# Performance work log

Measured on AMD Instinct MI355X. Metric: run time of the kernel, lower is better.

The kernel has to match this reference:

```python
import jax, jax.numpy as jnp
import numpy as np
import math

# Model hyperparameters (SchNet defaults)
H = 128        # hidden_channels
F = 128        # num_filters
G = 50         # num_gaussians
CUT = 6.0      # cutoff (Angstrom)
L_INT = 3      # num_interactions
# Graph scale
N_MOL = 512    # molecules
APM = 32       # atoms per molecule
N = N_MOL * APM
BOX = 10.0     # side of cubic box per molecule


def _ssp(x):
    # ShiftedSoftplus
    return jax.nn.softplus(x) - math.log(2.0)


def setup_inputs() -> dict:
    rng = np.random.default_rng(0)
    pos = rng.uniform(0.0, BOX, (N_MOL, APM, 3)).astype(np.float32)
    # radius graph within each molecule (faithful to radius_graph_custom,
    # precomputed here because edge count is data-dependent)
    srcs, dsts = [], []
    for m in range(N_MOL):
        p = pos[m]
        dm = np.linalg.norm(p[:, None, :] - p[None, :, :], axis=-1)
        mask = dm <= CUT
        np.fill_diagonal(mask, False)
        s, t = np.nonzero(mask)
        srcs.append(s + m * APM)
        dsts.append(t + m * APM)
    edge_index = np.stack([np.concatenate(srcs), np.concatenate(dsts)]).astype(np.int32)
    pos = pos.reshape(N, 3)
    batch = np.repeat(np.arange(N_MOL, dtype=np.int32), APM)
    z = rng.integers(1, 100, N).astype(np.int32)

    key = jax.random.key(0)
    ks = jax.random.split(key, 16)
    s = 0.1
    nrm = lambda k, shp: (jax.random.normal(k, shp, dtype=jnp.float32) * s)
    return {
        "z": jnp.asarray(z),
        "pos": jnp.asarray(pos),
        "batch": jnp.asarray(batch),
        "edge_index": jnp.asarray(edge_index),
        "emb": nrm(ks[0], (100, H)),
        "mlp_w1": nrm(ks[1], (L_INT, G, F)),
        "mlp_b1": jnp.zeros((L_INT, F), jnp.float32),
        "mlp_w2": nrm(ks[2], (L_INT, F, F)),
        "mlp_b2": jnp.zeros((L_INT, F), jnp.float32),
        "cf1_w": nrm(ks[3], (L_INT, H, F)),
        "cf2_w": nrm(ks[4], (L_INT, F, H)),
        "cf2_b": jnp.zeros((L_INT, H), jnp.float32),
        "lin_w": nrm(ks[5], (L_INT, H, H)),
        "lin_b": jnp.zeros((L_INT, H), jnp.float32),
        "out1_w": nrm(ks[6], (H, H // 2)),
        "out1_b": jnp.zeros((H // 2,), jnp.float32),
        "out2_w": nrm(ks[7], (H // 2, 1)),
        "out2_b": jnp.zeros((1,), jnp.float32),
    }


def reference(z, pos, batch, edge_index, emb,
              mlp_w1, mlp_b1, mlp_w2, mlp_b2,
              cf1_w, cf2_w, cf2_b, lin_w, lin_b,
              out1_w, out1_b, out2_w, out2_b):
    src, dst = edge_index[0], edge_index[1]
    # edge_weight = euclidean distance (== cdist[src, dst])
    d = jnp.sqrt(jnp.sum((pos[src] - pos[dst]) ** 2, axis=-1))  # [E]
    # GaussianSmearing
    offs = jnp.linspace(0.0, CUT, G)
    coeff = -0.5 / (CUT / (G - 1)) ** 2
    edge_attr = jnp.exp(coeff * (d[:, None] - offs[None, :]) ** 2)  # [E, G]
    # cosine cutoff
    Ccut = 0.5 * (jnp.cos(d * math.pi / CUT) + 1.0)  # [E]

    h = emb[z]  # [N, H]
    for l in range(L_INT):
        # edge filter MLP with cutoff
        W = _ssp(edge_attr @ mlp_w1[l] + mlp_b1[l]) @ mlp_w2[l] + mlp_b2[l]  # [E, F]
        W = W * Ccut[:, None]
        # CFConv: lin1 -> gather x_j -> multiply -> scatter-add to dst -> lin2
        msg = (h @ cf1_w[l])[src] * W                                # [E, F]
        agg = jax.ops.segment_sum(msg, dst, num_segments=N)          # [N, F]
        v = agg @ cf2_w[l] + cf2_b[l]                                # [N, H]
        v = _ssp(v)
        v = v @ lin_w[l] + lin_b[l]
        h = h + v  # residual

    h = _ssp(h @ out1_w + out1_b)
    h = h @ out2_w + out2_b                                          # [N, 1]
    out = jax.ops.segment_sum(h, batch, num_segments=N_MOL)          # [N_MOL, 1]
    return out
```

## Files before the change

kernel.cpp:

```cpp
#include <hip/hip_runtime.h>
#include <hip/hip_bf16.h>
#include <math.h>

#define NATOMS 16384
#define NMOL   512
#define APM    32
#define GDIM   50
#define KTAB   4096
#define MAXEPM 1000

#define STRH 132
#define STRA 136

typedef __attribute__((ext_vector_type(8))) short   short8;
typedef __attribute__((ext_vector_type(4))) float   floatx4;

__device__ __forceinline__ float ssp(float x) {
    float e = __expf(-fabsf(x));
    return fmaxf(x, 0.0f) + __logf(1.0f + e) - 0.69314718055994531f;
}

__device__ __forceinline__ unsigned short f2bf(float x) {
    union { float f; unsigned int u; } v; v.f = x;
    unsigned int lsb = (v.u >> 16) & 1u;
    v.u += 0x7fffu + lsb;
    return (unsigned short)(v.u >> 16);
}

__device__ __forceinline__ unsigned int pk2bf(float a, float b) {
    __hip_bfloat162 h = __float22bfloat162_rn(make_float2(a, b));
    unsigned int u;
    __builtin_memcpy(&u, &h, 4);
    return u;
}

#define KW1 72
#define KW2 136
#define NTILE (KTAB / 64)

__global__ __launch_bounds__(256) void mega_setup_kernel(
    const float* __restrict__ pos, const int* __restrict__ eidx, int E, int EB,
    int* __restrict__ rowptr,
    const float* __restrict__ cf1, const float* __restrict__ cf2,
    const float* __restrict__ lin, const float* __restrict__ out1,
    unsigned short* __restrict__ Wtall, unsigned int* __restrict__ meta,
    const float* __restrict__ w1_, const float* __restrict__ b1_,
    const float* __restrict__ w2_, const float* __restrict__ b2_,
    unsigned short* __restrict__ Tt)
{
    const int WB = (9 * 16384 + 64 * 128 + 255) / 256;
    const int b = blockIdx.x;
    const int tid = threadIdx.x;

    if (b < EB) {
        int idx = b * 256 + tid;
        if (idx < E) {
            int s = eidx[idx], t = eidx[E + idx];
            float dx = pos[3 * s]     - pos[3 * t];
            float dy = pos[3 * s + 1] - pos[3 * t + 1];
            float dz = pos[3 * s + 2] - pos[3 * t + 2];
            float d  = sqrtf(dx * dx + dy * dy + dz * dz);
            float u  = d * (float)(KTAB - 1) / 6.0f;
            int i = min((int)(u + 0.5f), KTAB - 1);
            meta[idx] = ((unsigned)i << 6) | (unsigned)(t & 31);
        } else if (idx < E + NATOMS + 1) {
            int a = idx - E;
            int lo = 0, hi = E;
            while (lo < hi) { int mid = (lo + hi) >> 1; if (eidx[mid] < a) lo = mid + 1; else hi = mid; }
            rowptr[a] = lo;
        }
        return;
    }
    if (b < EB + WB) {
        int idx = (b - EB) * 256 + tid;
        if (idx < 9 * 16384) {
            int wi = idx >> 14, rem = idx & 16383;
            int n = rem >> 7, k = rem & 127;
            int l = wi / 3, which = wi % 3;
            const float* src = (which == 0) ? cf1 : (which == 1) ? cf2 : lin;
            Wtall[idx] = f2bf(src[(size_t)l * 16384 + k * 128 + n]);
        } else if (idx < 9 * 16384 + 64 * 128) {
            int q = idx - 9 * 16384;
            int n = q >> 7, k = q & 127;
            Wtall[idx] = f2bf(out1[k * 64 + n]);
        }
        return;
    }

    __shared__ unsigned short s_bufA[128 * KW2];
    __shared__ unsigned short s_bufB[128 * KW1];

    const int tt = b - EB - WB;
    const int l  = tt / NTILE;
    const int bx = tt % NTILE;
    const float* w1 = w1_ + (size_t)l * GDIM * 128;
    const float* b1 = b1_ + (size_t)l * 128;
    const float* w2 = w2_ + (size_t)l * 128 * 128;
    const float* b2 = b2_ + (size_t)l * 128;
    unsigned short* Tg = Tt + (size_t)l * KTAB * 128;

    unsigned short* s_w1T = s_bufB;
    unsigned short* s_w2T = s_bufA;
    unsigned short* s_t   = s_bufB;

    for (int i = tid; i < GDIM * 128; i += 256) {
        int g = i >> 7, f = i & 127;
        s_w1T[f * KW1 + g] = f2bf(w1[i]);
    }
    for (int i = tid; i < (64 - GDIM) * 128; i += 256) {
        int g = GDIM + (i >> 7), f = i & 127;
        s_w1T[f * KW1 + g] = 0;
    }
    for (int i = tid; i < 128 * 128; i += 256) {
        int k = i >> 7, n = i & 127;
        s_w2T[n * KW2 + k] = f2bf(w2[i]);
    }

    const int lane = tid & 63;
    const int w    = tid >> 6;
    const int l15  = lane & 15;
    const int quad = lane >> 4;

    float b1v[8], b2v[8];
    #pragma unroll
    for (int nt = 0; nt < 8; nt++) {
        b1v[nt] = b1[nt * 16 + l15];
        b2v[nt] = b2[nt * 16 + l15];
    }
    __syncthreads();

    const float hstep = 6.0f / (float)(KTAB - 1);
    const float step  = 6.0f / 49.0f;
    const float coeff = -0.5f / (step * step);
    const float pioc  = 3.14159265358979323846f / 6.0f;
    const int k0 = bx * 64;
    const float dm = (float)(k0 + w * 16 + l15) * hstep;

    floatx4 acc1[8];
    #pragma unroll
    for (int nt = 0; nt < 8; nt++) acc1[nt] = (floatx4){0.f, 0.f, 0.f, 0.f};
    #pragma unroll
    for (int ks = 0; ks < 2; ks++) {
        unsigned int ap[4];
        #pragma unroll
        for (int jj = 0; jj < 4; jj++) {
            int g0 = ks * 32 + quad * 8 + 2 * jj;
            float d0 = dm - (float)g0 * step;
            float d1 = dm - (float)(g0 + 1) * step;
            float v0 = (g0 < GDIM)     ? __expf(coeff * d0 * d0) : 0.0f;
            float v1 = (g0 + 1 < GDIM) ? __expf(coeff * d1 * d1) : 0.0f;
            ap[jj] = pk2bf(v0, v1);
        }
        short8 af;
        __builtin_memcpy(&af, ap, 16);
        #pragma unroll
        for (int nt = 0; nt < 8; nt++) {
            short8 bfg = *(const short8*)&s_w1T[(nt * 16 + l15) * KW1 + ks * 32 + quad * 8];
            acc1[nt] = __builtin_amdgcn_mfma_f32_16x16x32_bf16(af, bfg, acc1[nt], 0, 0, 0);
        }
    }
    __syncthreads();

    #pragma unroll
    for (int nt = 0; nt < 8; nt++) {
        #pragma unroll
        for (int r = 0; r < 4; r++) {
            int row = w * 16 + quad * 4 + r;
            s_t[row * KW2 + nt * 16 + l15] = f2bf(ssp(acc1[nt][r] + b1v[nt]));
        }
    }

    floatx4 acc2[8];
    #pragma unroll
    for (int nt = 0; nt < 8; nt++) acc2[nt] = (floatx4){0.f, 0.f, 0.f, 0.f};
    #pragma unroll
    for (int ks = 0; ks < 4; ks++) {
        short8 af = *(const short8*)&s_t[(w * 16 + l15) * KW2 + ks * 32 + quad * 8];
        #pragma unroll
        for (int nt = 0; nt < 8; nt++) {
            short8 bfg = *(const short8*)&s_w2T[(nt * 16 + l15) * KW2 + ks * 32 + quad * 8];
            acc2[nt] = __builtin_amdgcn_mfma_f32_16x16x32_bf16(af, bfg, acc2[nt], 0, 0, 0);
        }
    }

    #pragma unroll
    for (int nt = 0; nt < 8; nt++) {
        #pragma unroll
        for (int r = 0; r < 4; r++) {
            int row = w * 16 + quad * 4 + r;
            float d = (float)(k0 + row) * hstep;
            float cut = 0.5f * (__cosf(d * pioc) + 1.0f);
            Tg[(size_t)(k0 + row) * 128 + nt * 16 + l15] = f2bf((acc2[nt][r] + b2v[nt]) * cut);
        }
    }
}

__global__ __launch_bounds__(512, 4) void fused_schnet_kernel(
    const int* __restrict__ z, const float* __restrict__ emb,
    const int* __restrict__ rowptr, const unsigned int* __restrict__ meta,
    const unsigned short* __restrict__ Tt,
    const unsigned short* __restrict__ Wtall,
    const float* __restrict__ cf2_b, const float* __restrict__ lin_b,
    const float* __restrict__ out1_b, const float* __restrict__ out2_w,
    const float* __restrict__ out2_b,
    float* __restrict__ out)
{
    __shared__ float s_h[32 * STRH];
    __shared__ float s_hx[33 * 128];
    __shared__ unsigned short s_agg[32 * STRA];
    __shared__ unsigned int s_meta[MAXEPM];
    __shared__ float s_red;
    unsigned short* s_t = (unsigned short*)s_hx;

    const int tid  = threadIdx.x;
    const int lane = tid & 63;
    const int w    = tid >> 6;
    const int l15  = lane & 15;
    const int quad = lane >> 4;
    const int r16  = (w & 1) * 16;
    const int c32  = (w >> 1) * 32;
    const int B0   = blockIdx.x * 32;

    for (int i = tid; i < 32 * 128; i += 512) {
        int row = i >> 7, col = i & 127;
        s_h[row * STRH + col] = emb[(size_t)z[B0 + row] * 128 + col];
    }
    if (tid < 128) s_hx[32 * 128 + tid] = 0.0f;
    if (tid == 0) s_red = 0.0f;

    const int ebase = rowptr[B0];
    const int nE    = rowptr[B0 + 32] - ebase;
    for (int i = tid; i < nE; i += 512) s_meta[i] = meta[ebase + i];
    if (tid == 0) s_meta[nE] = 32u;

    const int rp = rowptr[B0 + w * 4 + min(lane, 4)] - ebase;

    const unsigned short* WtO = Wtall + 9 * 16384;

    for (int l = 0; l < 3; l++) {
        const unsigned short* W1 = Wtall + (size_t)(l * 3 + 0) * 16384;
        const unsigned short* W2 = Wtall + (size_t)(l * 3 + 1) * 16384;
        const unsigned short* W3 = Wtall + (size_t)(l * 3 + 2) * 16384;
        const unsigned short* Ttl = Tt + (size_t)l * KTAB * 128;

        __syncthreads();

        floatx4 acc[2];
        #pragma unroll
        for (int nt = 0; nt < 2; nt++) acc[nt] = (floatx4){0.f, 0.f, 0.f, 0.f};
        #pragma unroll
        for (int ks = 0; ks < 4; ks++) {
            const float* hp = &s_h[(r16 + l15) * STRH + ks * 32 + quad * 8];
            float4 xa = *(const float4*)hp;
            float4 xb = *(const float4*)(hp + 4);
            unsigned int ap[4];
            ap[0] = pk2bf(xa.x, xa.y); ap[1] = pk2bf(xa.z, xa.w);
            ap[2] = pk2bf(xb.x, xb.y); ap[3] = pk2bf(xb.z, xb.w);
            short8 af;
            __builtin_memcpy(&af, ap, 16);
            #pragma unroll
            for (int nt = 0; nt < 2; nt++) {
                short8 bfg = *(const short8*)&W1[(size_t)(c32 + nt * 16 + l15) * 128 + ks * 32 + quad * 8];
                acc[nt] = __builtin_amdgcn_mfma_f32_16x16x32_bf16(af, bfg, acc[nt], 0, 0, 0);
            }
        }
        #pragma unroll
        for (int nt = 0; nt < 2; nt++) {
            #pragma unroll
            for (int r = 0; r < 4; r++)
                s_hx[(r16 + quad * 4 + r) * 128 + c32 + nt * 16 + l15] = acc[nt][r];
        }

        __syncthreads();

        for (int al = 0; al < 4; al++) {
            const int e0 = __shfl(rp, al);
            const int e1 = __shfl(rp, al + 1);
            float ax[8], ay[8];
            #pragma unroll
            for (int j = 0; j < 8; j++) { ax[j] = 0.f; ay[j] = 0.f; }
            for (int e = e0; e < e1; e += 8) {
                #pragma unroll
                for (int j = 0; j < 8; j++) {
                    int idx = (e + j < e1) ? (e + j) : nE;
                    unsigned int q = s_meta[idx];
                    int tl   = q & 63;
                    int knot = q >> 6;
                    unsigned int tp = *(const unsigned int*)&Ttl[((size_t)knot << 7) + 2 * lane];
                    float2 hv = *(const float2*)&s_hx[(tl << 7) + 2 * lane];
                    ax[j] = fmaf(hv.x, __uint_as_float(tp << 16), ax[j]);
                    ay[j] = fmaf(hv.y, __uint_as_float(tp & 0xffff0000u), ay[j]);
                }
            }
            float sx = ((ax[0] + ax[1]) + (ax[2] + ax[3])) + ((ax[4] + ax[5]) + (ax[6] + ax[7]));
            float sy = ((ay[0] + ay[1]) + (ay[2] + ay[3])) + ((ay[4] + ay[5]) + (ay[6] + ay[7]));
            *(unsigned int*)&s_agg[(w * 4 + al) * STRA + 2 * lane] = pk2bf(sx, sy);
        }

        __syncthreads();

        float bva[2], bvb[2];
        #pragma unroll
        for (int nt = 0; nt < 2; nt++) {
            bva[nt] = cf2_b[l * 128 + c32 + nt * 16 + l15];
            bvb[nt] = lin_b[l * 128 + c32 + nt * 16 + l15];
        }
        #pragma unroll
        for (int nt = 0; nt < 2; nt++) acc[nt] = (floatx4){0.f, 0.f, 0.f, 0.f};
        #pragma unroll
        for (int ks = 0; ks < 4; ks++) {
            short8 af = *(const short8*)&s_agg[(r16 + l15) * STRA + ks * 32 + quad * 8];
            #pragma unroll
            for (int nt = 0; nt < 2; nt++) {
                short8 bfg = *(const short8*)&W2[(size_t)(c32 + nt * 16 + l15) * 128 + ks * 32 + quad * 8];
                acc[nt] = __builtin_amdgcn_mfma_f32_16x16x32_bf16(af, bfg, acc[nt], 0, 0, 0);
            }
        }
        #pragma unroll
        for (int nt = 0; nt < 2; nt++) {
            #pragma unroll
            for (int r = 0; r < 4; r++) {
                int row = r16 + quad * 4 + r;
                s_t[row * STRA + c32 + nt * 16 + l15] = f2bf(ssp(acc[nt][r] + bva[nt]));
            }
        }

        __syncthreads();

        #pragma unroll
        for (int nt = 0; nt < 2; nt++) acc[nt] = (floatx4){0.f, 0.f, 0.f, 0.f};
        #pragma unroll
        for (int ks = 0; ks < 4; ks++) {
            short8 af = *(const short8*)&s_t[(r16 + l15) * STRA + ks * 32 + quad * 8];
            #pragma unroll
            for (int nt = 0; nt < 2; nt++) {
                short8 bfg = *(const short8*)&W3[(size_t)(c32 + nt * 16 + l15) * 128 + ks * 32 + quad * 8];
                acc[nt] = __builtin_amdgcn_mfma_f32_16x16x32_bf16(af, bfg, acc[nt], 0, 0, 0);
            }
        }
        #pragma unroll
        for (int nt = 0; nt < 2; nt++) {
            #pragma unroll
            for (int r = 0; r < 4; r++) {
                int row = r16 + quad * 4 + r;
                s_h[row * STRH + c32 + nt * 16 + l15] += acc[nt][r] + bvb[nt];
            }
        }
    }

    __syncthreads();

    const int c16 = (w >> 1) * 16;
    floatx4 ha = (floatx4){0.f, 0.f, 0.f, 0.f};
    #pragma unroll
    for (int ks = 0; ks < 4; ks++) {
        const float* hp = &s_h[(r16 + l15) * STRH + ks * 32 + quad * 8];
        float4 xa = *(const float4*)hp;
        float4 xb = *(const float4*)(hp + 4);
        unsigned int ap[4];
        ap[0] = pk2bf(xa.x, xa.y); ap[1] = pk2bf(xa.z, xa.w);
        ap[2] = pk2bf(xb.x, xb.y); ap[3] = pk2bf(xb.z, xb.w);
        short8 af;
        __builtin_memcpy(&af, ap, 16);
        short8 bfg = *(const short8*)&WtO[(size_t)(c16 + l15) * 128 + ks * 32 + quad * 8];
        ha = __builtin_amdgcn_mfma_f32_16x16x32_bf16(af, bfg, ha, 0, 0, 0);
    }
    float part = 0.0f;
    {
        float b1o = out1_b[c16 + l15];
        float o2  = out2_w[c16 + l15];
        #pragma unroll
        for (int r = 0; r < 4; r++)
            part += ssp(ha[r] + b1o) * o2;
    }
    #pragma unroll
    for (int off = 32; off > 0; off >>= 1) part += __shfl_down(part, off);
    if (lane == 0) atomicAdd(&s_red, part);
    __syncthreads();
    if (tid == 0) out[blockIdx.x] = s_red + 32.0f * out2_b[0];
}

extern "C" void kernel_launch(void* const* d_in, const int* in_sizes, int n_in,
                              void* d_out, int out_size, void* d_ws, size_t ws_size,
                              hipStream_t stream)
{
    const int*   z      = (const int*)d_in[0];
    const float* pos    = (const float*)d_in[1];
    const int*   eidx   = (const int*)d_in[3];
    const float* emb    = (const float*)d_in[4];
    const float* mlp_w1 = (const float*)d_in[5];
    const float* mlp_b1 = (const float*)d_in[6];
    const float* mlp_w2 = (const float*)d_in[7];
    const float* mlp_b2 = (const float*)d_in[8];
    const float* cf1_w  = (const float*)d_in[9];
    const float* cf2_w  = (const float*)d_in[10];
    const float* cf2_b  = (const float*)d_in[11];
    const float* lin_w  = (const float*)d_in[12];
    const float* lin_b  = (const float*)d_in[13];
    const float* out1_w = (const float*)d_in[14];
    const float* out1_b = (const float*)d_in[15];
    const float* out2_w = (const float*)d_in[16];
    const float* out2_b = (const float*)d_in[17];
    const int E = in_sizes[3] / 2;

    char* p = (char*)d_ws;
    unsigned int* meta = (unsigned int*)p;        p += ((size_t)(E + 1) * 4 + 63) & ~63ULL;
    unsigned short* Tt = (unsigned short*)p;      p += (size_t)3 * KTAB * 128 * 2;
    int* rowptr = (int*)p;                        p += ((size_t)(NATOMS + 1) * 4 + 63) & ~63ULL;
    unsigned short* Wtall = (unsigned short*)p;

    const int EB = (E + NATOMS + 1 + 255) / 256;
    const int WB = (9 * 16384 + 64 * 128 + 255) / 256;
    const int TB = NTILE * 3;
    mega_setup_kernel<<<EB + WB + TB, 256, 0, stream>>>(
        pos, eidx, E, EB, rowptr, cf1_w, cf2_w, lin_w, out1_w, Wtall, meta,
        mlp_w1, mlp_b1, mlp_w2, mlp_b2, Tt);

    fused_schnet_kernel<<<NMOL, 512, 0, stream>>>(
        z, emb, rowptr, meta, Tt, Wtall,
        cf2_b, lin_b, out1_b, out2_w, out2_b, (float*)d_out);
}
```

Before: 169.1 us.

## Split setup into weight pre-conversion pass and LUT-build kernel reading global bf16

The single mega setup kernel is split into two launches. The first converts the edge-filter MLP weights to bf16 in the transposed layout the MFMA wants, alongside the existing edge metadata, rowptr and linear-weight conversion. The second builds the distance lookup table, reading the B operands directly from global/L2 instead of having every tile block redo the fp32 conversion and transposed LDS staging. This removes per-block redundant conversion work and two barriers, at the cost of an extra kernel launch and a dependency between the two setup stages.

```diff
diff --git a/kernel.cpp b/kernel.cpp
--- a/kernel.cpp
+++ b/kernel.cpp
@@ -34,88 +34,85 @@
     return u;
 }
 
-#define KW1 72
-#define KW2 136
-#define NTILE (KTAB / 64)
-
-__global__ __launch_bounds__(256) void mega_setup_kernel(
-    const float* __restrict__ pos, const int* __restrict__ eidx, int E, int EB,
+__global__ __launch_bounds__(256) void setup1_kernel(
+    const float* __restrict__ pos, const int* __restrict__ eidx, int E,
     int* __restrict__ rowptr,
     const float* __restrict__ cf1, const float* __restrict__ cf2,
     const float* __restrict__ lin, const float* __restrict__ out1,
+    const float* __restrict__ w1_, const float* __restrict__ w2_,
     unsigned short* __restrict__ Wtall, unsigned int* __restrict__ meta,
-    const float* __restrict__ w1_, const float* __restrict__ b1_,
-    const float* __restrict__ w2_, const float* __restrict__ b2_,
+    unsigned short* __restrict__ Wm1, unsigned short* __restrict__ Wm2)
+{
+    int idx = blockIdx.x * 256 + threadIdx.x;
+    if (idx < E) {
+        int s = eidx[idx], t = eidx[E + idx];
+        float dx = pos[3 * s]     - pos[3 * t];
+        float dy = pos[3 * s + 1] - pos[3 * t + 1];
+        float dz = pos[3 * s + 2] - pos[3 * t + 2];
+        float d  = sqrtf(dx * dx + dy * dy + dz * dz);
+        float u  = d * (float)(KTAB - 1) / 6.0f;
+        int i = min((int)(u + 0.5f), KTAB - 1);
+        meta[idx] = ((unsigned)i << 6) | (unsigned)(t & 31);
+        return;
+    }
+    idx -= E;
+    if (idx < NATOMS + 1) {
+        int a = idx;
+        int lo = 0, hi = E;
+        while (lo < hi) { int mid = (lo + hi) >> 1; if (eidx[mid] < a) lo = mid + 1; else hi = mid; }
+        rowptr[a] = lo;
+        return;
+    }
+    idx -= NATOMS + 1;
+    if (idx < 9 * 16384) {
+        int wi = idx >> 14, rem = idx & 16383;
+        int n = rem >> 7, k = rem & 127;
+        int l = wi / 3, which = wi % 3;
+        const float* src = (which == 0) ? cf1 : (which == 1) ? cf2 : lin;
+        Wtall[idx] = f2bf(src[(size_t)l * 16384 + k * 128 + n]);
+        return;
+    }
+    idx -= 9 * 16384;
+    if (idx < 64 * 128) {
+        int n = idx >> 7, k = idx & 127;
+        Wtall[9 * 16384 + idx] = f2bf(out1[k * 64 + n]);
+        return;
+    }
+    idx -= 64 * 128;
+    if (idx < 3 * 128 * 64) {
+        int l = idx / 8192, rem = idx % 8192;
+        int n = rem >> 6, g = rem & 63;
+        Wm1[idx] = (g < GDIM) ? f2bf(w1_[(size_t)l * GDIM * 128 + g * 128 + n]) : 0;
+        return;
+    }
+    idx -= 3 * 128 * 64;
+    if (idx < 3 * 128 * 128) {
+        int l = idx / 16384, rem = idx % 16384;
+        int n = rem >> 7, k = rem & 127;
+        Wm2[idx] = f2bf(w2_[(size_t)l * 16384 + k * 128 + n]);
+        return;
+    }
+}
+
+#define KW2 136
+#define NTILE (KTAB / 64)
+
+__global__ __launch_bounds__(256) void setup2_kernel(
+    const unsigned short* __restrict__ Wm1, const unsigned short* __restrict__ Wm2,
+    const float* __restrict__ b1_, const float* __restrict__ b2_,
     unsigned short* __restrict__ Tt)
 {
-    const int WB = (9 * 16384 + 64 * 128 + 255) / 256;
-    const int b = blockIdx.x;
-    const int tid = threadIdx.x;
-
-    if (b < EB) {
-        int idx = b * 256 + tid;
-        if (idx < E) {
-            int s = eidx[idx], t = eidx[E + idx];
-            float dx = pos[3 * s]     - pos[3 * t];
-            float dy = pos[3 * s + 1] - pos[3 * t + 1];
-            float dz = pos[3 * s + 2] - pos[3 * t + 2];
-            float d  = sqrtf(dx * dx + dy * dy + dz * dz);
-            float u  = d * (float)(KTAB - 1) / 6.0f;
-            int i = min((int)(u + 0.5f), KTAB - 1);
-            meta[idx] = ((unsigned)i << 6) | (unsigned)(t & 31);
-        } else if (idx < E + NATOMS + 1) {
-            int a = idx - E;
-            int lo = 0, hi = E;
-            while (lo < hi) { int mid = (lo + hi) >> 1; if (eidx[mid] < a) lo = mid + 1; else hi = mid; }
-            rowptr[a] = lo;
-        }
-        return;
-    }
-    if (b < EB + WB) {
-        int idx = (b - EB) * 256 + tid;
-        if (idx < 9 * 16384) {
-            int wi = idx >> 14, rem = idx & 16383;
-            int n = rem >> 7, k = rem & 127;
-            int l = wi / 3, which = wi % 3;
-            const float* src = (which == 0) ? cf1 : (which == 1) ? cf2 : lin;
-            Wtall[idx] = f2bf(src[(size_t)l * 16384 + k * 128 + n]);
-        } else if (idx < 9 * 16384 + 64 * 128) {
-            int q = idx - 9 * 16384;
-            int n = q >> 7, k = q & 127;
-            Wtall[idx] = f2bf(out1[k * 64 + n]);
-        }
-        return;
-    }
-
-    __shared__ unsigned short s_bufA[128 * KW2];
-    __shared__ unsigned short s_bufB[128 * KW1];
-
-    const int tt = b - EB - WB;
-    const int l  = tt / NTILE;
-    const int bx = tt % NTILE;
-    const float* w1 = w1_ + (size_t)l * GDIM * 128;
+    __shared__ unsigned short s_t[64 * KW2];
+
+    const int bx = blockIdx.x;
+    const int l  = blockIdx.y;
+    const unsigned short* W1m = Wm1 + (size_t)l * 128 * 64;
+    const unsigned short* W2m = Wm2 + (size_t)l * 128 * 128;
     const float* b1 = b1_ + (size_t)l * 128;
-    const float* w2 = w2_ + (size_t)l * 128 * 128;
     const float* b2 = b2_ + (size_t)l * 128;
     unsigned short* Tg = Tt + (size_t)l * KTAB * 128;
 
-    unsigned short* s_w1T = s_bufB;
-    unsigned short* s_w2T = s_bufA;
-    unsigned short* s_t   = s_bufB;
-
-    for (int i = tid; i < GDIM * 128; i += 256) {
-        int g = i >> 7, f = i & 127;
-        s_w1T[f * KW1 + g] = f2bf(w1[i]);
-    }
-    for (int i = tid; i < (64 - GDIM) * 128; i += 256) {
-        int g = GDIM + (i >> 7), f = i & 127;
-        s_w1T[f * KW1 + g] = 0;
-    }
-    for (int i = tid; i < 128 * 128; i += 256) {
-        int k = i >> 7, n = i & 127;
-        s_w2T[n * KW2 + k] = f2bf(w2[i]);
-    }
-
+    const int tid  = threadIdx.x;
     const int lane = tid & 63;
     const int w    = tid >> 6;
     const int l15  = lane & 15;
@@ -127,7 +124,6 @@
         b1v[nt] = b1[nt * 16 + l15];
         b2v[nt] = b2[nt * 16 + l15];
     }
-    __syncthreads();
 
     const float hstep = 6.0f / (float)(KTAB - 1);
     const float step  = 6.0f / 49.0f;
@@ -155,12 +151,10 @@
         __builtin_memcpy(&af, ap, 16);
         #pragma unroll
         for (int nt = 0; nt < 8; nt++) {
-            short8 bfg = *(const short8*)&s_w1T[(nt * 16 + l15) * KW1 + ks * 32 + quad * 8];
+            short8 bfg = *(const short8*)&W1m[(size_t)(nt * 16 + l15) * 64 + ks * 32 + quad * 8];
             acc1[nt] = __builtin_amdgcn_mfma_f32_16x16x32_bf16(af, bfg, acc1[nt], 0, 0, 0);
         }
     }
-    __syncthreads();
-
     #pragma unroll
     for (int nt = 0; nt < 8; nt++) {
         #pragma unroll
@@ -178,7 +172,7 @@
         short8 af = *(const short8*)&s_t[(w * 16 + l15) * KW2 + ks * 32 + quad * 8];
         #pragma unroll
         for (int nt = 0; nt < 8; nt++) {
-            short8 bfg = *(const short8*)&s_w2T[(nt * 16 + l15) * KW2 + ks * 32 + quad * 8];
+            short8 bfg = *(const short8*)&W2m[(size_t)(nt * 16 + l15) * 128 + ks * 32 + quad * 8];
             acc2[nt] = __builtin_amdgcn_mfma_f32_16x16x32_bf16(af, bfg, acc2[nt], 0, 0, 0);
         }
     }
@@ -407,14 +401,18 @@
     unsigned int* meta = (unsigned int*)p;        p += ((size_t)(E + 1) * 4 + 63) & ~63ULL;
     unsigned short* Tt = (unsigned short*)p;      p += (size_t)3 * KTAB * 128 * 2;
     int* rowptr = (int*)p;                        p += ((size_t)(NATOMS + 1) * 4 + 63) & ~63ULL;
-    unsigned short* Wtall = (unsigned short*)p;
-
-    const int EB = (E + NATOMS + 1 + 255) / 256;
-    const int WB = (9 * 16384 + 64 * 128 + 255) / 256;
-    const int TB = NTILE * 3;
-    mega_setup_kernel<<<EB + WB + TB, 256, 0, stream>>>(
-        pos, eidx, E, EB, rowptr, cf1_w, cf2_w, lin_w, out1_w, Wtall, meta,
-        mlp_w1, mlp_b1, mlp_w2, mlp_b2, Tt);
+    unsigned short* Wtall = (unsigned short*)p;   p += (size_t)(9 * 16384 + 64 * 128) * 2;
+    unsigned short* Wm1 = (unsigned short*)p;     p += (size_t)3 * 128 * 64 * 2;
+    unsigned short* Wm2 = (unsigned short*)p;
+
+    const int total1 = E + (NATOMS + 1) + 9 * 16384 + 64 * 128
+                     + 3 * 128 * 64 + 3 * 128 * 128;
+    setup1_kernel<<<(total1 + 255) / 256, 256, 0, stream>>>(
+        pos, eidx, E, rowptr, cf1_w, cf2_w, lin_w, out1_w,
+        mlp_w1, mlp_w2, Wtall, meta, Wm1, Wm2);
+
+    setup2_kernel<<<dim3(NTILE, 3), 256, 0, stream>>>(
+        Wm1, Wm2, mlp_b1, mlp_b2, Tt);
 
     fused_schnet_kernel<<<NMOL, 512, 0, stream>>>(
         z, emb, rowptr, meta, Tt, Wtall,
```

Result: slower. 173.1 us (+2.3%).
